# Performance work log

Hardware: AMD Instinct MI355X
Metric: run time of the kernel (lower is better)

## Reference

```python
import jax, jax.numpy as jnp
import numpy as np

IN_DIMS = (32, 64, 96, 128)
N_EXPERTS = len(IN_DIMS)
MAX_F = max(IN_DIMS)
D = 2 * MAX_F
N = 8192
TOP_K = 2
H_DIM = 1024
OUT_DIM = 768
LN_EPS = 1e-6


def _build_mask():
    # mask[f] = [1]*s + [0]*(MAX_F-s) + [1]*s + [0]*(MAX_F-s), shape (E, 1, D)
    m = np.zeros((N_EXPERTS, 1, D), dtype=np.float32)
    for i, s in enumerate(IN_DIMS):
        m[i, 0, :s] = 1.0
        m[i, 0, MAX_F:MAX_F + s] = 1.0
    return jnp.asarray(m)

_MASK = _build_mask()


def _multi_in_expert(x_final, expert_weights, expert_indices, W, b):
    """MoE dispatch/combine of MultiInSizeLinear (expert_indices path).
    x_final: (E, N, D); expert_weights/indices: (N, K); W: (E, O, D); b: (E, O)."""
    Wm = W * _MASK                                   # (E, O, D) masked per-size weights
    # per-expert outputs for every token (the torch loop computes these per mask group)
    Y = jnp.einsum('end,eod->eno', x_final, Wm) + b[:, None, :]   # (E, N, O)
    valid = expert_indices < N_EXPERTS               # (N, K) real-expert mask
    rsum = jnp.sum(expert_weights * valid, axis=-1, keepdims=True)
    rsum = jnp.where(rsum == 0, 1.0, rsum)
    wnorm = jnp.where(valid, expert_weights / rsum, 0.0)          # (N, K)
    safe = jnp.where(valid, expert_indices, 0)
    n_idx = jnp.arange(Y.shape[1])
    gathered = Y[safe, n_idx[:, None]]               # (N, K, O)
    return jnp.sum(wnorm[..., None] * gathered, axis=1)           # (N, O)


def setup_inputs() -> dict:
    key = jax.random.key(0)
    ks = jax.random.split(key, 12)
    s_hid = 1.0 / np.sqrt(D)
    s_out = 1.0 / np.sqrt(H_DIM)
    return {
        'x': jax.random.normal(ks[0], (N, D), jnp.float32),
        'in_feat_size': jax.random.randint(ks[1], (N,), 0, MAX_F, jnp.int64) if jax.config.jax_enable_x64 else jax.random.randint(ks[1], (N,), 0, MAX_F, jnp.int32),
        'expert_weights': jax.random.uniform(ks[2], (N, TOP_K), jnp.float32),
        'expert_indices': jax.random.randint(ks[3], (N, TOP_K), 0, 6, jnp.int32),
        'x_final': jax.random.normal(ks[4], (N_EXPERTS, N, D), jnp.float32),
        'W_hid': jax.random.normal(ks[5], (N_EXPERTS, H_DIM, D), jnp.float32) * s_hid,
        'b_hid': jax.random.normal(ks[6], (N_EXPERTS, H_DIM), jnp.float32) * s_hid,
        'W_out': jax.random.normal(ks[7], (OUT_DIM, H_DIM), jnp.float32) * s_out,
        'b_out': jax.random.normal(ks[8], (OUT_DIM,), jnp.float32) * s_out,
        'W_res': jax.random.normal(ks[9], (N_EXPERTS, OUT_DIM, D), jnp.float32) * s_hid,
        'b_res': jax.random.normal(ks[10], (N_EXPERTS, OUT_DIM), jnp.float32) * s_hid,
        'ln_w': jnp.ones((OUT_DIM,), jnp.float32),
    }


def reference(x, in_feat_size, expert_weights, expert_indices, x_final,
              W_hid, b_hid, W_out, b_out, W_res, b_res, ln_w):
    xf = jnp.nan_to_num(x_final, nan=0.0)
    hid = _multi_in_expert(xf, expert_weights, expert_indices, W_hid, b_hid)
    hid = jax.nn.gelu(hid, approximate=False)
    out = hid @ W_out.T + b_out                      # output_layer (dropout p=0 -> identity)
    res = _multi_in_expert(xf, expert_weights, expert_indices, W_res, b_res)
    out = out + res
    # T5LayerNorm (RMSNorm)
    var = jnp.mean(out * out, axis=-1, keepdims=True)
    return ln_w * (out * jax.lax.rsqrt(var + LN_EPS))
```

## Files before the change

### kernel.cpp

```cpp
#include <hip/hip_runtime.h>
#include <hip/hip_bf16.h>

#define TOKENS 8192
#define D_IN   256
#define HDIM   1024
#define ODIM   768
#define KPACK  704
#define NCHUNK 88

typedef short bf16x8 __attribute__((ext_vector_type(8)));
typedef float f32x4  __attribute__((ext_vector_type(4)));

static __device__ __forceinline__ ushort f2b(float f) {
    union { __hip_bfloat16 b; ushort u; } cv;
    cv.b = __float2bfloat16(f);
    return cv.u;
}
static __device__ __forceinline__ float b2f(ushort u) {
    union { ushort u; __hip_bfloat16 b; } cv;
    cv.u = u;
    return __bfloat162float(cv.b);
}

static __device__ __forceinline__ void chunk_map(int c8, int& e, int& d0) {
    int cc;
    if (c8 < 8)       { e = 0; cc = c8; }
    else if (c8 < 24) { e = 1; cc = c8 - 8; }
    else if (c8 < 48) { e = 2; cc = c8 - 24; }
    else              { e = 3; cc = c8 - 48; }
    int half = 4 * (e + 1);
    d0 = (cc < half) ? cc * 8 : 128 + (cc - half) * 8;
}

static __device__ __forceinline__ void stage16(const ushort* g, ushort* l) {
    __builtin_amdgcn_global_load_lds(
        (const __attribute__((address_space(1))) void*)g,
        (__attribute__((address_space(3))) void*)l, 16, 0, 0);
}

static __device__ __forceinline__ float gelu_f(float v) {
    float y = 0.7978845608f * v * (1.f + 0.044715f * v * v);
    return v - v / (__expf(2.f * y) + 1.f);
}

#define A_ITEMS  (TOKENS * NCHUNK)
#define B_ITEMS  (1792 * NCHUNK)
#define W_ITEMS  (768 * 128)
__global__ __launch_bounds__(256) void k_pack(
    const float* __restrict__ ew, const int* __restrict__ ei,
    const float* __restrict__ xf,
    const float* __restrict__ Whid, const float* __restrict__ bhid,
    const float* __restrict__ Wres, const float* __restrict__ bres,
    const float* __restrict__ Wout,
    ushort* __restrict__ Ap, ushort* __restrict__ Bp, ushort* __restrict__ Wb) {
    int gid = blockIdx.x * 256 + threadIdx.x;
    if (gid < A_ITEMS) {
        int n  = gid / NCHUNK;
        int c8 = gid - n * NCHUNK;
        int   i0 = ei[2 * n], i1 = ei[2 * n + 1];
        float w0 = ew[2 * n], w1 = ew[2 * n + 1];
        bool v0 = (unsigned)i0 < 4u, v1 = (unsigned)i1 < 4u;
        float rs = (v0 ? w0 : 0.f) + (v1 ? w1 : 0.f);
        if (rs == 0.f) rs = 1.f;
        float o0 = v0 ? w0 / rs : 0.f;
        float o1 = v1 ? w1 / rs : 0.f;
        ushort o[8] __attribute__((aligned(16))) = {0, 0, 0, 0, 0, 0, 0, 0};
        if (c8 < 80) {
            int e, d0;
            chunk_map(c8, e, d0);
            float w = ((v0 && i0 == e) ? o0 : 0.f) + ((v1 && i1 == e) ? o1 : 0.f);
            if (w != 0.f) {
                const float* s = xf + ((size_t)e * TOKENS + n) * D_IN + d0;
#pragma unroll
                for (int j = 0; j < 8; ++j) {
                    float v = s[j];
                    if (!(v == v)) v = 0.f;
                    o[j] = f2b(w * v);
                }
            }
        } else if (c8 == 80) {
#pragma unroll
            for (int j = 0; j < 4; ++j) {
                float m = ((v0 && i0 == j) ? o0 : 0.f) + ((v1 && i1 == j) ? o1 : 0.f);
                o[j] = f2b(m);
            }
        }
        *(uint4*)(Ap + (size_t)n * KPACK + c8 * 8) = *(const uint4*)o;
    } else if (gid < A_ITEMS + B_ITEMS) {
        int g2 = gid - A_ITEMS;
        int o_ = g2 / NCHUNK;
        int c8 = g2 - o_ * NCHUNK;
        ushort v[8] __attribute__((aligned(16))) = {0, 0, 0, 0, 0, 0, 0, 0};
        if (c8 < 80) {
            int e, d0;
            chunk_map(c8, e, d0);
            const float* s = (o_ < HDIM)
                ? Whid + ((size_t)e * HDIM + o_) * D_IN + d0
                : Wres + ((size_t)e * ODIM + (o_ - HDIM)) * D_IN + d0;
#pragma unroll
            for (int j = 0; j < 8; ++j) v[j] = f2b(s[j]);
        } else if (c8 == 80) {
#pragma unroll
            for (int j = 0; j < 4; ++j) {
                float b = (o_ < HDIM) ? bhid[j * HDIM + o_] : bres[j * ODIM + (o_ - HDIM)];
                v[j] = f2b(b);
            }
        }
        *(uint4*)(Bp + (size_t)o_ * KPACK + c8 * 8) = *(const uint4*)v;
    } else {
        int g3 = gid - A_ITEMS - B_ITEMS;
        const float* s = Wout + (size_t)g3 * 8;
        ushort v[8] __attribute__((aligned(16)));
#pragma unroll
        for (int j = 0; j < 8; ++j) v[j] = f2b(s[j]);
        *(uint4*)(Wb + (size_t)g3 * 8) = *(const uint4*)v;
    }
}

__global__ __launch_bounds__(256, 2) void k_gemm1(
    const ushort* __restrict__ A, const ushort* __restrict__ B,
    ushort* __restrict__ hidB, ushort* __restrict__ resb) {
    __shared__ __align__(16) ushort As[2][128 * 64];
    __shared__ __align__(16) ushort Bs[2][128 * 64];
    const int tid = threadIdx.x;
    const int lane = tid & 63, w = tid >> 6;
    const int wr = w >> 1, wc = w & 1;
    const int r = lane & 15, g = lane >> 4;

    int bid  = blockIdx.x;
    int widx = (bid & 7) * 112 + (bid >> 3);
    int bm = widx / 14, bn = widx - bm * 14;

    const int srow = tid >> 3;
    const int gc   = (tid & 7) ^ (srow & 7);
    const ushort* Ag = A + (size_t)(bm * 128 + srow) * KPACK + gc * 8;
    const ushort* Bg = B + (size_t)(bn * 128 + srow) * KPACK + gc * 8;
    const int ldst = (w * 8) * 64;

#define G1_STAGE(p, kt) do {                                            \
    _Pragma("unroll")                                                   \
    for (int i_ = 0; i_ < 4; ++i_) {                                    \
        stage16(Ag + (size_t)(i_ * 32) * KPACK + (kt), &As[p][ldst + i_ * 32 * 64]); \
        stage16(Bg + (size_t)(i_ * 32) * KPACK + (kt), &Bs[p][ldst + i_ * 32 * 64]); \
    } } while (0)

    G1_STAGE(0, 0);
    G1_STAGE(1, 64);

    f32x4 acc[4][4] = {};
    const int cA = (wr * 64 + r) * 64;
    const int cB = (wc * 64 + r) * 64;
    const int sx = r & 7;
    const int cs0 = ((0 * 4 + g) ^ sx) * 8;
    const int cs1 = ((1 * 4 + g) ^ sx) * 8;

    int cur = 0;
#pragma unroll
    for (int t = 0; t < 11; ++t) {
        if (t < 10) asm volatile("s_waitcnt vmcnt(8)" ::: "memory");
        else        asm volatile("s_waitcnt vmcnt(0)" ::: "memory");
        __builtin_amdgcn_s_barrier();
        const ushort* Ab = As[cur];
        const ushort* Bb = Bs[cur];
        bf16x8 a0[4], b0[4], a1[4], b1[4];
#pragma unroll
        for (int j = 0; j < 4; ++j) {
            b0[j] = *(const bf16x8*)&Bb[cB + j * 16 * 64 + cs0];
            b1[j] = *(const bf16x8*)&Bb[cB + j * 16 * 64 + cs1];
        }
#pragma unroll
        for (int i = 0; i < 4; ++i) {
            a0[i] = *(const bf16x8*)&Ab[cA + i * 16 * 64 + cs0];
            a1[i] = *(const bf16x8*)&Ab[cA + i * 16 * 64 + cs1];
        }
        asm volatile("s_waitcnt lgkmcnt(0)" ::: "memory");
        __builtin_amdgcn_sched_barrier(0);
        __builtin_amdgcn_s_barrier();
        if (t + 2 < 11) G1_STAGE(cur, (t + 2) * 64);
        __builtin_amdgcn_s_setprio(1);
#pragma unroll
        for (int i = 0; i < 4; ++i)
#pragma unroll
            for (int j = 0; j < 4; ++j)
                acc[i][j] = __builtin_amdgcn_mfma_f32_16x16x32_bf16(
                    a0[i], b0[j], acc[i][j], 0, 0, 0);
#pragma unroll
        for (int i = 0; i < 4; ++i)
#pragma unroll
            for (int j = 0; j < 4; ++j)
                acc[i][j] = __builtin_amdgcn_mfma_f32_16x16x32_bf16(
                    a1[i], b1[j], acc[i][j], 0, 0, 0);
        __builtin_amdgcn_s_setprio(0);
        cur ^= 1;
    }
#undef G1_STAGE

    if (bn < 8) {
#pragma unroll
        for (int fi = 0; fi < 4; ++fi) {
#pragma unroll
            for (int j = 0; j < 4; ++j) {
                int col = bn * 128 + wc * 64 + j * 16 + r;
#pragma unroll
                for (int qq = 0; qq < 4; ++qq) {
                    int row = bm * 128 + wr * 64 + fi * 16 + g * 4 + qq;
                    hidB[(size_t)row * HDIM + col] = f2b(gelu_f(acc[fi][j][qq]));
                }
            }
        }
    } else {
#pragma unroll
        for (int fi = 0; fi < 4; ++fi) {
#pragma unroll
            for (int j = 0; j < 4; ++j) {
                int col = (bn - 8) * 128 + wc * 64 + j * 16 + r;
#pragma unroll
                for (int qq = 0; qq < 4; ++qq) {
                    int row = bm * 128 + wr * 64 + fi * 16 + g * 4 + qq;
                    resb[(size_t)row * ODIM + col] = f2b(acc[fi][j][qq]);
                }
            }
        }
    }
}

__global__ __launch_bounds__(256, 2) void k_gemm2(
    const ushort* __restrict__ A, const ushort* __restrict__ B,
    const float* __restrict__ bout, const ushort* __restrict__ resb,
    ushort* __restrict__ outb) {
    __shared__ __align__(16) ushort As[2][128 * 64];
    __shared__ __align__(16) ushort Bs[2][128 * 64];
    const int tid = threadIdx.x;
    const int lane = tid & 63, w = tid >> 6;
    const int wr = w >> 1, wc = w & 1;
    const int r = lane & 15, g = lane >> 4;
    const int bm = blockIdx.x, bn = blockIdx.y;

    const int srow = tid >> 3;
    const int gc   = (tid & 7) ^ (srow & 7);
    const ushort* Ag = A + (size_t)(bm * 128 + srow) * HDIM + gc * 8;
    const ushort* Bg = B + (size_t)(bn * 128 + srow) * HDIM + gc * 8;
    const int ldst = (w * 8) * 64;

#define G2_STAGE(p, kt) do {                                            \
    _Pragma("unroll")                                                   \
    for (int i_ = 0; i_ < 4; ++i_) {                                    \
        stage16(Ag + (size_t)(i_ * 32) * HDIM + (kt), &As[p][ldst + i_ * 32 * 64]); \
        stage16(Bg + (size_t)(i_ * 32) * HDIM + (kt), &Bs[p][ldst + i_ * 32 * 64]); \
    } } while (0)

    G2_STAGE(0, 0);
    G2_STAGE(1, 64);

    f32x4 acc[4][4] = {};
    const int cA = (wr * 64 + r) * 64;
    const int cB = (wc * 64 + r) * 64;
    const int sx = r & 7;
    const int cs0 = ((0 * 4 + g) ^ sx) * 8;
    const int cs1 = ((1 * 4 + g) ^ sx) * 8;

    int cur = 0;
#pragma unroll
    for (int t = 0; t < 16; ++t) {
        if (t < 15) asm volatile("s_waitcnt vmcnt(8)" ::: "memory");
        else        asm volatile("s_waitcnt vmcnt(0)" ::: "memory");
        __builtin_amdgcn_s_barrier();
        const ushort* Ab = As[cur];
        const ushort* Bb = Bs[cur];
        bf16x8 a0[4], b0[4], a1[4], b1[4];
#pragma unroll
        for (int j = 0; j < 4; ++j) {
            b0[j] = *(const bf16x8*)&Bb[cB + j * 16 * 64 + cs0];
            b1[j] = *(const bf16x8*)&Bb[cB + j * 16 * 64 + cs1];
        }
#pragma unroll
        for (int i = 0; i < 4; ++i) {
            a0[i] = *(const bf16x8*)&Ab[cA + i * 16 * 64 + cs0];
            a1[i] = *(const bf16x8*)&Ab[cA + i * 16 * 64 + cs1];
        }
        asm volatile("s_waitcnt lgkmcnt(0)" ::: "memory");
        __builtin_amdgcn_sched_barrier(0);
        __builtin_amdgcn_s_barrier();
        if (t + 2 < 16) G2_STAGE(cur, (t + 2) * 64);
        __builtin_amdgcn_s_setprio(1);
#pragma unroll
        for (int i = 0; i < 4; ++i)
#pragma unroll
            for (int j = 0; j < 4; ++j)
                acc[i][j] = __builtin_amdgcn_mfma_f32_16x16x32_bf16(
                    a0[i], b0[j], acc[i][j], 0, 0, 0);
#pragma unroll
        for (int i = 0; i < 4; ++i)
#pragma unroll
            for (int j = 0; j < 4; ++j)
                acc[i][j] = __builtin_amdgcn_mfma_f32_16x16x32_bf16(
                    a1[i], b1[j], acc[i][j], 0, 0, 0);
        __builtin_amdgcn_s_setprio(0);
        cur ^= 1;
    }
#undef G2_STAGE

#pragma unroll
    for (int fi = 0; fi < 4; ++fi) {
#pragma unroll
        for (int j = 0; j < 4; ++j) {
            int col = bn * 128 + wc * 64 + j * 16 + r;
#pragma unroll
            for (int qq = 0; qq < 4; ++qq) {
                int row = bm * 128 + wr * 64 + fi * 16 + g * 4 + qq;
                size_t idx = (size_t)row * ODIM + col;
                float v = acc[fi][j][qq] + bout[col] + b2f(resb[idx]);
                outb[idx] = f2b(v);
            }
        }
    }
}

__global__ __launch_bounds__(256) void k_rms(
    const ushort* __restrict__ outb, const float* __restrict__ lnw,
    float* __restrict__ out) {
    int row = blockIdx.x, t = threadIdx.x;
    const ushort* p = outb + (size_t)row * ODIM;
    float v0 = b2f(p[t]), v1 = b2f(p[t + 256]), v2 = b2f(p[t + 512]);
    float s = v0 * v0 + v1 * v1 + v2 * v2;
#pragma unroll
    for (int off = 32; off > 0; off >>= 1) s += __shfl_down(s, off, 64);
    __shared__ float ws4[4];
    if ((t & 63) == 0) ws4[t >> 6] = s;
    __syncthreads();
    float tot = ws4[0] + ws4[1] + ws4[2] + ws4[3];
    float sc = rsqrtf(tot * (1.f / 768.f) + 1e-6f);
    out[(size_t)row * ODIM + t]       = lnw[t]       * v0 * sc;
    out[(size_t)row * ODIM + t + 256] = lnw[t + 256] * v1 * sc;
    out[(size_t)row * ODIM + t + 512] = lnw[t + 512] * v2 * sc;
}

extern "C" void kernel_launch(void* const* d_in, const int* in_sizes, int n_in,
                              void* d_out, int out_size, void* d_ws, size_t ws_size,
                              hipStream_t stream) {
    const float* ew   = (const float*)d_in[2];
    const int*   ei   = (const int*)d_in[3];
    const float* xf   = (const float*)d_in[4];
    const float* Whid = (const float*)d_in[5];
    const float* bhid = (const float*)d_in[6];
    const float* Wout = (const float*)d_in[7];
    const float* bout = (const float*)d_in[8];
    const float* Wres = (const float*)d_in[9];
    const float* bres = (const float*)d_in[10];
    const float* lnw  = (const float*)d_in[11];

    char* ws = (char*)d_ws;
    ushort* Ap   = (ushort*)(ws);
    ushort* Bp   = (ushort*)(ws + 11534336);
    ushort* Wb   = (ushort*)(ws + 14057472);
    ushort* hidB = (ushort*)(ws + 15630336);
    ushort* resb = (ushort*)(ws + 32407552);
    ushort* outb = (ushort*)(ws + 44990464);

    k_pack<<<3816, 256, 0, stream>>>(ew, ei, xf, Whid, bhid, Wres, bres, Wout,
                                     Ap, Bp, Wb);
    k_gemm1<<<896, 256, 0, stream>>>(Ap, Bp, hidB, resb);
    k_gemm2<<<dim3(64, 6), 256, 0, stream>>>(hidB, Wb, bout, resb, outb);
    k_rms<<<8192, 256, 0, stream>>>(outb, lnw, (float*)d_out);
}
```

Before: 67.76 us.

## Load A operand directly from global into registers, stage only B in LDS

Both GEMM kernels stop staging the A tile through shared memory. Each wave now loads its own A fragments straight from global memory into a double-buffered register array one k-step ahead, while only B still goes through LDS. This halves LDS use and LDS traffic per block. In exchange it raises register pressure (16 more bf16x8 vectors), re-reads A rows redundantly across the two column waves, and moves the vmcnt waits to after the MFMA block, which may expose global latency.

```diff
diff --git a/kernel.cpp b/kernel.cpp
--- a/kernel.cpp
+++ b/kernel.cpp
@@ -120,12 +120,12 @@
 __global__ __launch_bounds__(256, 2) void k_gemm1(
     const ushort* __restrict__ A, const ushort* __restrict__ B,
     ushort* __restrict__ hidB, ushort* __restrict__ resb) {
-    __shared__ __align__(16) ushort As[2][128 * 64];
     __shared__ __align__(16) ushort Bs[2][128 * 64];
     const int tid = threadIdx.x;
     const int lane = tid & 63, w = tid >> 6;
     const int wr = w >> 1, wc = w & 1;
     const int r = lane & 15, g = lane >> 4;
+    const int sx = r & 7;
 
     int bid  = blockIdx.x;
     int widx = (bid & 7) * 112 + (bid >> 3);
@@ -133,67 +133,68 @@
 
     const int srow = tid >> 3;
     const int gc   = (tid & 7) ^ (srow & 7);
-    const ushort* Ag = A + (size_t)(bm * 128 + srow) * KPACK + gc * 8;
     const ushort* Bg = B + (size_t)(bn * 128 + srow) * KPACK + gc * 8;
     const int ldst = (w * 8) * 64;
-
-#define G1_STAGE(p, kt) do {                                            \
-    _Pragma("unroll")                                                   \
-    for (int i_ = 0; i_ < 4; ++i_) {                                    \
-        stage16(Ag + (size_t)(i_ * 32) * KPACK + (kt), &As[p][ldst + i_ * 32 * 64]); \
-        stage16(Bg + (size_t)(i_ * 32) * KPACK + (kt), &Bs[p][ldst + i_ * 32 * 64]); \
+    const ushort* Arow = A + (size_t)(bm * 128 + wr * 64 + r) * KPACK + g * 8;
+
+#define STAGE_B(p, t) do { _Pragma("unroll")                                 \
+    for (int i_ = 0; i_ < 4; ++i_)                                           \
+        stage16(Bg + (size_t)(i_ * 32) * KPACK + (t) * 64,                   \
+                &Bs[p][ldst + i_ * 32 * 64]); } while (0)
+#define LOAD_A(buf, t) do { _Pragma("unroll")                                \
+    for (int mi_ = 0; mi_ < 4; ++mi_) { _Pragma("unroll")                    \
+        for (int ks_ = 0; ks_ < 2; ++ks_)                                    \
+            areg[buf][ks_ * 4 + mi_] = *(const bf16x8*)(                     \
+                Arow + (size_t)(mi_ * 16) * KPACK + (t) * 64 + ks_ * 32);    \
     } } while (0)
 
-    G1_STAGE(0, 0);
-    G1_STAGE(1, 64);
+    bf16x8 areg[2][8];
+    STAGE_B(0, 0);
+    LOAD_A(0, 0);
+    __builtin_amdgcn_sched_barrier(0);
+    STAGE_B(1, 1);
+    asm volatile("s_waitcnt vmcnt(4)" ::: "memory");
+    __builtin_amdgcn_s_barrier();
 
     f32x4 acc[4][4] = {};
-    const int cA = (wr * 64 + r) * 64;
     const int cB = (wc * 64 + r) * 64;
-    const int sx = r & 7;
-    const int cs0 = ((0 * 4 + g) ^ sx) * 8;
-    const int cs1 = ((1 * 4 + g) ^ sx) * 8;
-
-    int cur = 0;
+
 #pragma unroll
     for (int t = 0; t < 11; ++t) {
-        if (t < 10) asm volatile("s_waitcnt vmcnt(8)" ::: "memory");
-        else        asm volatile("s_waitcnt vmcnt(0)" ::: "memory");
-        __builtin_amdgcn_s_barrier();
-        const ushort* Ab = As[cur];
-        const ushort* Bb = Bs[cur];
-        bf16x8 a0[4], b0[4], a1[4], b1[4];
-#pragma unroll
-        for (int j = 0; j < 4; ++j) {
-            b0[j] = *(const bf16x8*)&Bb[cB + j * 16 * 64 + cs0];
-            b1[j] = *(const bf16x8*)&Bb[cB + j * 16 * 64 + cs1];
-        }
-#pragma unroll
-        for (int i = 0; i < 4; ++i) {
-            a0[i] = *(const bf16x8*)&Ab[cA + i * 16 * 64 + cs0];
-            a1[i] = *(const bf16x8*)&Ab[cA + i * 16 * 64 + cs1];
-        }
-        asm volatile("s_waitcnt lgkmcnt(0)" ::: "memory");
+        const int cb = t & 1;
+        if (t + 1 < 11) LOAD_A((t + 1) & 1, t + 1);
         __builtin_amdgcn_sched_barrier(0);
-        __builtin_amdgcn_s_barrier();
-        if (t + 2 < 11) G1_STAGE(cur, (t + 2) * 64);
+        bf16x8 bf_[2][4];
+#pragma unroll
+        for (int ks = 0; ks < 2; ++ks)
+#pragma unroll
+            for (int j = 0; j < 4; ++j)
+                bf_[ks][j] = *(const bf16x8*)&Bs[cb][cB + j * 16 * 64 + (((ks * 4 + g) ^ sx) * 8)];
         __builtin_amdgcn_s_setprio(1);
 #pragma unroll
-        for (int i = 0; i < 4; ++i)
-#pragma unroll
-            for (int j = 0; j < 4; ++j)
-                acc[i][j] = __builtin_amdgcn_mfma_f32_16x16x32_bf16(
-                    a0[i], b0[j], acc[i][j], 0, 0, 0);
-#pragma unroll
-        for (int i = 0; i < 4; ++i)
-#pragma unroll
-            for (int j = 0; j < 4; ++j)
-                acc[i][j] = __builtin_amdgcn_mfma_f32_16x16x32_bf16(
-                    a1[i], b1[j], acc[i][j], 0, 0, 0);
+        for (int ks = 0; ks < 2; ++ks)
+#pragma unroll
+            for (int mi = 0; mi < 4; ++mi)
+#pragma unroll
+                for (int j = 0; j < 4; ++j)
+                    acc[mi][j] = __builtin_amdgcn_mfma_f32_16x16x32_bf16(
+                        areg[cb][ks * 4 + mi], bf_[ks][j], acc[mi][j], 0, 0, 0);
         __builtin_amdgcn_s_setprio(0);
-        cur ^= 1;
-    }
-#undef G1_STAGE
+        if (t + 1 < 11) {
+            asm volatile("s_waitcnt lgkmcnt(0)" ::: "memory");
+            __builtin_amdgcn_sched_barrier(0);
+            __builtin_amdgcn_s_barrier();
+            if (t + 2 < 11) {
+                STAGE_B(cb, t + 2);
+                asm volatile("s_waitcnt vmcnt(4)" ::: "memory");
+            } else {
+                asm volatile("s_waitcnt vmcnt(0)" ::: "memory");
+            }
+            __builtin_amdgcn_s_barrier();
+        }
+    }
+#undef STAGE_B
+#undef LOAD_A
 
     if (bn < 8) {
 #pragma unroll
@@ -228,77 +229,78 @@
     const ushort* __restrict__ A, const ushort* __restrict__ B,
     const float* __restrict__ bout, const ushort* __restrict__ resb,
     ushort* __restrict__ outb) {
-    __shared__ __align__(16) ushort As[2][128 * 64];
     __shared__ __align__(16) ushort Bs[2][128 * 64];
     const int tid = threadIdx.x;
     const int lane = tid & 63, w = tid >> 6;
     const int wr = w >> 1, wc = w & 1;
     const int r = lane & 15, g = lane >> 4;
+    const int sx = r & 7;
     const int bm = blockIdx.x, bn = blockIdx.y;
 
     const int srow = tid >> 3;
     const int gc   = (tid & 7) ^ (srow & 7);
-    const ushort* Ag = A + (size_t)(bm * 128 + srow) * HDIM + gc * 8;
     const ushort* Bg = B + (size_t)(bn * 128 + srow) * HDIM + gc * 8;
     const int ldst = (w * 8) * 64;
-
-#define G2_STAGE(p, kt) do {                                            \
-    _Pragma("unroll")                                                   \
-    for (int i_ = 0; i_ < 4; ++i_) {                                    \
-        stage16(Ag + (size_t)(i_ * 32) * HDIM + (kt), &As[p][ldst + i_ * 32 * 64]); \
-        stage16(Bg + (size_t)(i_ * 32) * HDIM + (kt), &Bs[p][ldst + i_ * 32 * 64]); \
+    const ushort* Arow = A + (size_t)(bm * 128 + wr * 64 + r) * HDIM + g * 8;
+
+#define STAGE_B(p, t) do { _Pragma("unroll")                                 \
+    for (int i_ = 0; i_ < 4; ++i_)                                           \
+        stage16(Bg + (size_t)(i_ * 32) * HDIM + (t) * 64,                    \
+                &Bs[p][ldst + i_ * 32 * 64]); } while (0)
+#define LOAD_A(buf, t) do { _Pragma("unroll")                                \
+    for (int mi_ = 0; mi_ < 4; ++mi_) { _Pragma("unroll")                    \
+        for (int ks_ = 0; ks_ < 2; ++ks_)                                    \
+            areg[buf][ks_ * 4 + mi_] = *(const bf16x8*)(                     \
+                Arow + (size_t)(mi_ * 16) * HDIM + (t) * 64 + ks_ * 32);     \
     } } while (0)
 
-    G2_STAGE(0, 0);
-    G2_STAGE(1, 64);
+    bf16x8 areg[2][8];
+    STAGE_B(0, 0);
+    LOAD_A(0, 0);
+    __builtin_amdgcn_sched_barrier(0);
+    STAGE_B(1, 1);
+    asm volatile("s_waitcnt vmcnt(4)" ::: "memory");
+    __builtin_amdgcn_s_barrier();
 
     f32x4 acc[4][4] = {};
-    const int cA = (wr * 64 + r) * 64;
     const int cB = (wc * 64 + r) * 64;
-    const int sx = r & 7;
-    const int cs0 = ((0 * 4 + g) ^ sx) * 8;
-    const int cs1 = ((1 * 4 + g) ^ sx) * 8;
-
-    int cur = 0;
+
 #pragma unroll
     for (int t = 0; t < 16; ++t) {
-        if (t < 15) asm volatile("s_waitcnt vmcnt(8)" ::: "memory");
-        else        asm volatile("s_waitcnt vmcnt(0)" ::: "memory");
-        __builtin_amdgcn_s_barrier();
-        const ushort* Ab = As[cur];
-        const ushort* Bb = Bs[cur];
-        bf16x8 a0[4], b0[4], a1[4], b1[4];
-#pragma unroll
-        for (int j = 0; j < 4; ++j) {
-            b0[j] = *(const bf16x8*)&Bb[cB + j * 16 * 64 + cs0];
-            b1[j] = *(const bf16x8*)&Bb[cB + j * 16 * 64 + cs1];
-        }
-#pragma unroll
-        for (int i = 0; i < 4; ++i) {
-            a0[i] = *(const bf16x8*)&Ab[cA + i * 16 * 64 + cs0];
-            a1[i] = *(const bf16x8*)&Ab[cA + i * 16 * 64 + cs1];
-        }
-        asm volatile("s_waitcnt lgkmcnt(0)" ::: "memory");
+        const int cb = t & 1;
+        if (t + 1 < 16) LOAD_A((t + 1) & 1, t + 1);
         __builtin_amdgcn_sched_barrier(0);
-        __builtin_amdgcn_s_barrier();
-        if (t + 2 < 16) G2_STAGE(cur, (t + 2) * 64);
+        bf16x8 bf_[2][4];
+#pragma unroll
+        for (int ks = 0; ks < 2; ++ks)
+#pragma unroll
+            for (int j = 0; j < 4; ++j)
+                bf_[ks][j] = *(const bf16x8*)&Bs[cb][cB + j * 16 * 64 + (((ks * 4 + g) ^ sx) * 8)];
         __builtin_amdgcn_s_setprio(1);
 #pragma unroll
-        for (int i = 0; i < 4; ++i)
-#pragma unroll
-            for (int j = 0; j < 4; ++j)
-                acc[i][j] = __builtin_amdgcn_mfma_f32_16x16x32_bf16(
-                    a0[i], b0[j], acc[i][j], 0, 0, 0);
-#pragma unroll
-        for (int i = 0; i < 4; ++i)
-#pragma unroll
-            for (int j = 0; j < 4; ++j)
-                acc[i][j] = __builtin_amdgcn_mfma_f32_16x16x32_bf16(
-                    a1[i], b1[j], acc[i][j], 0, 0, 0);
+        for (int ks = 0; ks < 2; ++ks)
+#pragma unroll
+            for (int mi = 0; mi < 4; ++mi)
+#pragma unroll
+                for (int j = 0; j < 4; ++j)
+                    acc[mi][j] = __builtin_amdgcn_mfma_f32_16x16x32_bf16(
+                        areg[cb][ks * 4 + mi], bf_[ks][j], acc[mi][j], 0, 0, 0);
         __builtin_amdgcn_s_setprio(0);
-        cur ^= 1;
-    }
-#undef G2_STAGE
+        if (t + 1 < 16) {
+            asm volatile("s_waitcnt lgkmcnt(0)" ::: "memory");
+            __builtin_amdgcn_sched_barrier(0);
+            __builtin_amdgcn_s_barrier();
+            if (t + 2 < 16) {
+                STAGE_B(cb, t + 2);
+                asm volatile("s_waitcnt vmcnt(4)" ::: "memory");
+            } else {
+                asm volatile("s_waitcnt vmcnt(0)" ::: "memory");
+            }
+            __builtin_amdgcn_s_barrier();
+        }
+    }
+#undef STAGE_B
+#undef LOAD_A
 
 #pragma unroll
     for (int fi = 0; fi < 4; ++fi) {
```

Result: slower. 114.4 us (+68.8%).
